# Performance work log

Measured on AMD Instinct MI355X. Metric: run time of the kernel, lower is better.

Reference implementation:

```python
import jax, jax.numpy as jnp
import numpy as np

IN_FEATURES = 4096
OUT_FEATURES = 4096
BLOCK_SIZE = 16
E2M1_VALUES = jnp.array([0.0, 0.5, 1.0, 1.5, 2.0, 3.0, 4.0, 6.0], dtype=jnp.float32)


def dequantize_nvfp4(weight_packed, weight_scales, out_features, in_features, block_size, dtype):
    # Unpack two 4-bit codes per byte: even positions = high nibble, odd = low nibble
    p = weight_packed.astype(jnp.int32)
    high = (p >> 4) & 15
    low = p & 15
    unpacked = jnp.stack([high, low], axis=-1).reshape(-1)  # [out*in]
    sign = ((unpacked >> 3) & 1).astype(dtype)
    mag_code = unpacked & 7
    magnitude = E2M1_VALUES.astype(dtype)[mag_code]
    vals = jnp.where(sign == 1, -magnitude, magnitude)
    # Expand per-block E4M3 scales (repeat_interleave)
    scales_expanded = jnp.repeat(weight_scales.astype(dtype), block_size)
    w = vals * scales_expanded
    return w.reshape(out_features, in_features)


def setup_inputs() -> dict:
    key = jax.random.key(0)
    k1, k2, k3, k4 = jax.random.split(key, 4)
    x = jax.random.normal(k1, (4, 2048, IN_FEATURES), dtype=jnp.float32)
    weight_packed = jax.random.randint(k2, (OUT_FEATURES * IN_FEATURES // 2,), 0, 256, dtype=jnp.int32)
    weight_scales = jax.random.uniform(k3, (OUT_FEATURES * IN_FEATURES // BLOCK_SIZE,), dtype=jnp.float32)
    bias = jax.random.normal(k4, (OUT_FEATURES,), dtype=jnp.float32)
    return {"x": x, "weight_packed": weight_packed, "weight_scales": weight_scales, "bias": bias}


def reference(x, weight_packed, weight_scales, bias):
    w = dequantize_nvfp4(weight_packed, weight_scales, OUT_FEATURES, IN_FEATURES, BLOCK_SIZE, x.dtype)
    # F.linear: y = x @ w.T + bias
    return jnp.einsum('bsi,oi->bso', x, w) + bias
```

## Files before the change

### kernel.cpp

```cpp
#include <hip/hip_runtime.h>
#include <cstdint>
#include <cstddef>

#define MDIM 8192
#define NDIM 4096
#define KDIM 4096

typedef __attribute__((ext_vector_type(8))) __bf16 bf16x8;
typedef __attribute__((ext_vector_type(4))) float floatx4;

typedef __attribute__((address_space(3))) void lds_t;
typedef __attribute__((address_space(1))) void glb_t;

__device__ __forceinline__ unsigned short f32_to_bf16(float f) {
  unsigned int u = __float_as_uint(f);
  u += 0x7FFFu + ((u >> 16) & 1u);
  return (unsigned short)(u >> 16);
}

__device__ __forceinline__ float fp4_mag(int c) {
  int e = (c >> 1) & 3, m = c & 1;
  int sh = e ? (e - 1) : 0;
  return e ? 0.5f * (float)((2 + m) << sh) : 0.5f * (float)m;
}

__global__ __launch_bounds__(256) void conv_x_kernel(const float* __restrict__ x,
                                                     unsigned short* __restrict__ xb) {
  const int t = blockIdx.x * 256 + threadIdx.x;
  const float4* src = (const float4*)x + (size_t)t * 2;
  float4 a = src[0], b = src[1];
  union { unsigned short us[8]; uint4 u4; } o;
  o.us[0] = f32_to_bf16(a.x); o.us[1] = f32_to_bf16(a.y);
  o.us[2] = f32_to_bf16(a.z); o.us[3] = f32_to_bf16(a.w);
  o.us[4] = f32_to_bf16(b.x); o.us[5] = f32_to_bf16(b.y);
  o.us[6] = f32_to_bf16(b.z); o.us[7] = f32_to_bf16(b.w);
  ((uint4*)xb)[t] = o.u4;
}

__global__ __launch_bounds__(256) void dequant_kernel(const int* __restrict__ packed,
                                                      const float* __restrict__ scales,
                                                      unsigned short* __restrict__ wb) {
  const int t = blockIdx.x * 256 + threadIdx.x;
  const int4* p = (const int4*)packed + (size_t)t * 2;
  int4 pa = p[0], pb = p[1];
  float s = scales[t];
  int bytes[8] = {pa.x, pa.y, pa.z, pa.w, pb.x, pb.y, pb.z, pb.w};
  union { unsigned short us[16]; uint4 u4[2]; } o;
#pragma unroll
  for (int i = 0; i < 8; ++i) {
    int by = bytes[i] & 255;
    int hi = by >> 4, lo = by & 15;
    float vh = fp4_mag(hi & 7) * s; if (hi & 8) vh = -vh;
    float vl = fp4_mag(lo & 7) * s; if (lo & 8) vl = -vl;
    o.us[2 * i]     = f32_to_bf16(vh);
    o.us[2 * i + 1] = f32_to_bf16(vl);
  }
  uint4* dst = (uint4*)(wb + (size_t)t * 16);
  dst[0] = o.u4[0]; dst[1] = o.u4[1];
}

__global__ __launch_bounds__(256, 3) void gemm_kernel(const __bf16* __restrict__ A,
                                                      const __bf16* __restrict__ B,
                                                      const float* __restrict__ bias,
                                                      float* __restrict__ C) {
  __shared__ __bf16 As[128 * 32];
  __shared__ __bf16 Bs[128 * 32];
  const int t = threadIdx.x;
  const int wave = t >> 6, lane = t & 63;
  const int quad = lane >> 4, r16 = lane & 15;
  const int wm = (wave >> 1) * 64, wn = (wave & 1) * 64;
  const int m0 = blockIdx.y * 128, n0 = blockIdx.x * 128;

  floatx4 acc[4][4] = {};

  const int sr = t >> 2;
  const int sc = (t & 3) * 8;

  const __bf16* ga = A + (size_t)(m0 + sr) * KDIM + sc;
  const __bf16* gb = B + (size_t)(n0 + sr) * KDIM + sc;

  for (int k0 = 0; k0 < KDIM; k0 += 32) {
    __builtin_amdgcn_global_load_lds((const glb_t*)(ga),
                                     (lds_t*)(As + wave * 512), 16, 0, 0);
    __builtin_amdgcn_global_load_lds((const glb_t*)(ga + (size_t)64 * KDIM),
                                     (lds_t*)(As + 2048 + wave * 512), 16, 0, 0);
    __builtin_amdgcn_global_load_lds((const glb_t*)(gb),
                                     (lds_t*)(Bs + wave * 512), 16, 0, 0);
    __builtin_amdgcn_global_load_lds((const glb_t*)(gb + (size_t)64 * KDIM),
                                     (lds_t*)(Bs + 2048 + wave * 512), 16, 0, 0);
    ga += 32; gb += 32;
    __syncthreads();

    bf16x8 af[4], bfr[4];
#pragma unroll
    for (int i = 0; i < 4; ++i) {
      af[i]  = *(const bf16x8*)(As + (wm + i * 16 + r16) * 32 + quad * 8);
      bfr[i] = *(const bf16x8*)(Bs + (wn + i * 16 + r16) * 32 + quad * 8);
    }
#pragma unroll
    for (int i = 0; i < 4; ++i)
#pragma unroll
      for (int j = 0; j < 4; ++j)
        acc[i][j] = __builtin_amdgcn_mfma_f32_16x16x32_bf16(af[i], bfr[j], acc[i][j], 0, 0, 0);
    __syncthreads();
  }

  float bv[4];
#pragma unroll
  for (int j = 0; j < 4; ++j) bv[j] = bias[n0 + wn + j * 16 + r16];
#pragma unroll
  for (int i = 0; i < 4; ++i) {
    const int gm = m0 + wm + i * 16 + quad * 4;
#pragma unroll
    for (int j = 0; j < 4; ++j) {
      float* cp = C + (size_t)gm * NDIM + (n0 + wn + j * 16 + r16);
#pragma unroll
      for (int r = 0; r < 4; ++r)
        cp[(size_t)r * NDIM] = acc[i][j][r] + bv[j];
    }
  }
}

__global__ __launch_bounds__(256) void fused_fallback(const float* __restrict__ x,
                                                      const int* __restrict__ packed,
                                                      const float* __restrict__ scales,
                                                      const float* __restrict__ bias,
                                                      float* __restrict__ out) {
  const int n = blockIdx.x * 256 + threadIdx.x;
  const int m = blockIdx.y;
  const float* xr = x + (size_t)m * KDIM;
  const int* pr = packed + (size_t)n * (KDIM / 2);
  const float* sc = scales + (size_t)n * (KDIM / 16);
  float acc = 0.f;
  for (int kb = 0; kb < KDIM / 16; ++kb) {
    float s = sc[kb];
    float part = 0.f;
#pragma unroll
    for (int i = 0; i < 8; ++i) {
      int by = pr[kb * 8 + i] & 255;
      int hi = by >> 4, lo = by & 15;
      float vh = fp4_mag(hi & 7); if (hi & 8) vh = -vh;
      float vl = fp4_mag(lo & 7); if (lo & 8) vl = -vl;
      part += xr[kb * 16 + 2 * i] * vh + xr[kb * 16 + 2 * i + 1] * vl;
    }
    acc += s * part;
  }
  out[(size_t)m * NDIM + n] = acc + bias[n];
}

extern "C" void kernel_launch(void* const* d_in, const int* in_sizes, int n_in,
                              void* d_out, int out_size, void* d_ws, size_t ws_size,
                              hipStream_t stream) {
  const float* x      = (const float*)d_in[0];
  const int*   packed = (const int*)d_in[1];
  const float* scales = (const float*)d_in[2];
  const float* bias   = (const float*)d_in[3];
  float* out = (float*)d_out;

  const size_t needA = (size_t)MDIM * KDIM * 2;
  const size_t needW = (size_t)NDIM * KDIM * 2;

  if (ws_size >= needA + needW) {
    unsigned short* xb = (unsigned short*)d_ws;
    unsigned short* wb = (unsigned short*)((char*)d_ws + needA);
    conv_x_kernel<<<(MDIM * KDIM / 8) / 256, 256, 0, stream>>>(x, xb);
    dequant_kernel<<<(NDIM * KDIM / 16) / 256, 256, 0, stream>>>(packed, scales, wb);
    dim3 grid(NDIM / 128, MDIM / 128);
    gemm_kernel<<<grid, 256, 0, stream>>>((const __bf16*)xb, (const __bf16*)wb, bias, out);
  } else {
    dim3 grid(NDIM / 256, MDIM);
    fused_fallback<<<grid, 256, 0, stream>>>(x, packed, scales, bias, out);
  }
}
```

Measured before the change: 546.8 us.

## Switch GEMM to 32x32x16 MFMA tiles and merge prep kernels into one launch

The GEMM now uses 32x32x16 bf16 MFMA instructions with a 2x2 accumulator grid per wave instead of 4x4 16x16x32 tiles. This cuts the number of MFMA issues and LDS fragment loads per K step. The x conversion and weight dequant kernels are merged into a single launch, and each thread now handles twice as much data, which removes one kernel launch. The 32x32 output layout changes the store pattern, giving less coalesced writes per lane row.

```diff
diff --git a/kernel.cpp b/kernel.cpp
--- a/kernel.cpp
+++ b/kernel.cpp
@@ -7,7 +7,7 @@
 #define KDIM 4096
 
 typedef __attribute__((ext_vector_type(8))) __bf16 bf16x8;
-typedef __attribute__((ext_vector_type(4))) float floatx4;
+typedef __attribute__((ext_vector_type(16))) float floatx16;
 
 typedef __attribute__((address_space(3))) void lds_t;
 typedef __attribute__((address_space(1))) void glb_t;
@@ -24,39 +24,47 @@
   return e ? 0.5f * (float)((2 + m) << sh) : 0.5f * (float)m;
 }
 
-__global__ __launch_bounds__(256) void conv_x_kernel(const float* __restrict__ x,
-                                                     unsigned short* __restrict__ xb) {
-  const int t = blockIdx.x * 256 + threadIdx.x;
-  const float4* src = (const float4*)x + (size_t)t * 2;
-  float4 a = src[0], b = src[1];
-  union { unsigned short us[8]; uint4 u4; } o;
-  o.us[0] = f32_to_bf16(a.x); o.us[1] = f32_to_bf16(a.y);
-  o.us[2] = f32_to_bf16(a.z); o.us[3] = f32_to_bf16(a.w);
-  o.us[4] = f32_to_bf16(b.x); o.us[5] = f32_to_bf16(b.y);
-  o.us[6] = f32_to_bf16(b.z); o.us[7] = f32_to_bf16(b.w);
-  ((uint4*)xb)[t] = o.u4;
-}
-
-__global__ __launch_bounds__(256) void dequant_kernel(const int* __restrict__ packed,
-                                                      const float* __restrict__ scales,
-                                                      unsigned short* __restrict__ wb) {
-  const int t = blockIdx.x * 256 + threadIdx.x;
-  const int4* p = (const int4*)packed + (size_t)t * 2;
-  int4 pa = p[0], pb = p[1];
-  float s = scales[t];
-  int bytes[8] = {pa.x, pa.y, pa.z, pa.w, pb.x, pb.y, pb.z, pb.w};
-  union { unsigned short us[16]; uint4 u4[2]; } o;
+__global__ __launch_bounds__(256) void prep_kernel(const float* __restrict__ x,
+                                                   unsigned short* __restrict__ xb,
+                                                   const int* __restrict__ packed,
+                                                   const float* __restrict__ scales,
+                                                   unsigned short* __restrict__ wb) {
+  if (blockIdx.x < 8192) {
+    const int t = blockIdx.x * 256 + threadIdx.x;
+    const float4* src = (const float4*)x + (size_t)t * 4;
+    float4 a = src[0], b = src[1], c = src[2], d = src[3];
+    union { unsigned short us[16]; uint4 u4[2]; } o;
+    o.us[0]  = f32_to_bf16(a.x); o.us[1]  = f32_to_bf16(a.y);
+    o.us[2]  = f32_to_bf16(a.z); o.us[3]  = f32_to_bf16(a.w);
+    o.us[4]  = f32_to_bf16(b.x); o.us[5]  = f32_to_bf16(b.y);
+    o.us[6]  = f32_to_bf16(b.z); o.us[7]  = f32_to_bf16(b.w);
+    o.us[8]  = f32_to_bf16(c.x); o.us[9]  = f32_to_bf16(c.y);
+    o.us[10] = f32_to_bf16(c.z); o.us[11] = f32_to_bf16(c.w);
+    o.us[12] = f32_to_bf16(d.x); o.us[13] = f32_to_bf16(d.y);
+    o.us[14] = f32_to_bf16(d.z); o.us[15] = f32_to_bf16(d.w);
+    uint4* dst = (uint4*)xb + (size_t)t * 2;
+    dst[0] = o.u4[0]; dst[1] = o.u4[1];
+  } else {
+    const int u = (blockIdx.x - 8192) * 256 + threadIdx.x;
+    const int4* p = (const int4*)packed + (size_t)u * 4;
+    int4 p0 = p[0], p1 = p[1], p2 = p[2], p3 = p[3];
+    float s0 = scales[2 * u], s1 = scales[2 * u + 1];
+    int bytes[16] = {p0.x, p0.y, p0.z, p0.w, p1.x, p1.y, p1.z, p1.w,
+                     p2.x, p2.y, p2.z, p2.w, p3.x, p3.y, p3.z, p3.w};
+    union { unsigned short us[32]; uint4 u4[4]; } o;
 #pragma unroll
-  for (int i = 0; i < 8; ++i) {
-    int by = bytes[i] & 255;
-    int hi = by >> 4, lo = by & 15;
-    float vh = fp4_mag(hi & 7) * s; if (hi & 8) vh = -vh;
-    float vl = fp4_mag(lo & 7) * s; if (lo & 8) vl = -vl;
-    o.us[2 * i]     = f32_to_bf16(vh);
-    o.us[2 * i + 1] = f32_to_bf16(vl);
+    for (int i = 0; i < 16; ++i) {
+      float s = (i < 8) ? s0 : s1;
+      int by = bytes[i] & 255;
+      int hi = by >> 4, lo = by & 15;
+      float vh = fp4_mag(hi & 7) * s; if (hi & 8) vh = -vh;
+      float vl = fp4_mag(lo & 7) * s; if (lo & 8) vl = -vl;
+      o.us[2 * i]     = f32_to_bf16(vh);
+      o.us[2 * i + 1] = f32_to_bf16(vl);
+    }
+    uint4* dst = (uint4*)wb + (size_t)u * 4;
+    dst[0] = o.u4[0]; dst[1] = o.u4[1]; dst[2] = o.u4[2]; dst[3] = o.u4[3];
   }
-  uint4* dst = (uint4*)(wb + (size_t)t * 16);
-  dst[0] = o.u4[0]; dst[1] = o.u4[1];
 }
 
 __global__ __launch_bounds__(256, 3) void gemm_kernel(const __bf16* __restrict__ A,
@@ -67,11 +75,11 @@
   __shared__ __bf16 Bs[128 * 32];
   const int t = threadIdx.x;
   const int wave = t >> 6, lane = t & 63;
-  const int quad = lane >> 4, r16 = lane & 15;
+  const int r32 = lane & 31, half = lane >> 5;
   const int wm = (wave >> 1) * 64, wn = (wave & 1) * 64;
   const int m0 = blockIdx.y * 128, n0 = blockIdx.x * 128;
 
-  floatx4 acc[4][4] = {};
+  floatx16 acc[2][2] = {};
 
   const int sr = t >> 2;
   const int sc = (t & 3) * 8;
@@ -91,34 +99,37 @@
     ga += 32; gb += 32;
     __syncthreads();
 
-    bf16x8 af[4], bfr[4];
 #pragma unroll
-    for (int i = 0; i < 4; ++i) {
-      af[i]  = *(const bf16x8*)(As + (wm + i * 16 + r16) * 32 + quad * 8);
-      bfr[i] = *(const bf16x8*)(Bs + (wn + i * 16 + r16) * 32 + quad * 8);
+    for (int kh = 0; kh < 2; ++kh) {
+      bf16x8 af[2], bfr[2];
+#pragma unroll
+      for (int i = 0; i < 2; ++i) {
+        af[i]  = *(const bf16x8*)(As + (wm + i * 32 + r32) * 32 + kh * 16 + half * 8);
+        bfr[i] = *(const bf16x8*)(Bs + (wn + i * 32 + r32) * 32 + kh * 16 + half * 8);
+      }
+#pragma unroll
+      for (int i = 0; i < 2; ++i)
+#pragma unroll
+        for (int j = 0; j < 2; ++j)
+          acc[i][j] = __builtin_amdgcn_mfma_f32_32x32x16_bf16(af[i], bfr[j], acc[i][j], 0, 0, 0);
     }
-#pragma unroll
-    for (int i = 0; i < 4; ++i)
-#pragma unroll
-      for (int j = 0; j < 4; ++j)
-        acc[i][j] = __builtin_amdgcn_mfma_f32_16x16x32_bf16(af[i], bfr[j], acc[i][j], 0, 0, 0);
     __syncthreads();
   }
 
-  float bv[4];
+  float bv[2];
 #pragma unroll
-  for (int j = 0; j < 4; ++j) bv[j] = bias[n0 + wn + j * 16 + r16];
+  for (int j = 0; j < 2; ++j) bv[j] = bias[n0 + wn + j * 32 + r32];
 #pragma unroll
-  for (int i = 0; i < 4; ++i) {
-    const int gm = m0 + wm + i * 16 + quad * 4;
+  for (int i = 0; i < 2; ++i)
 #pragma unroll
-    for (int j = 0; j < 4; ++j) {
-      float* cp = C + (size_t)gm * NDIM + (n0 + wn + j * 16 + r16);
+    for (int j = 0; j < 2; ++j) {
+      const int gc = n0 + wn + j * 32 + r32;
 #pragma unroll
-      for (int r = 0; r < 4; ++r)
-        cp[(size_t)r * NDIM] = acc[i][j][r] + bv[j];
+      for (int r = 0; r < 16; ++r) {
+        const int gr = m0 + wm + i * 32 + (r & 3) + 8 * (r >> 2) + 4 * half;
+        C[(size_t)gr * NDIM + gc] = acc[i][j][r] + bv[j];
+      }
     }
-  }
 }
 
 __global__ __launch_bounds__(256) void fused_fallback(const float* __restrict__ x,
@@ -163,8 +174,7 @@
   if (ws_size >= needA + needW) {
     unsigned short* xb = (unsigned short*)d_ws;
     unsigned short* wb = (unsigned short*)((char*)d_ws + needA);
-    conv_x_kernel<<<(MDIM * KDIM / 8) / 256, 256, 0, stream>>>(x, xb);
-    dequant_kernel<<<(NDIM * KDIM / 16) / 256, 256, 0, stream>>>(packed, scales, wb);
+    prep_kernel<<<10240, 256, 0, stream>>>(x, xb, packed, scales, wb);
     dim3 grid(NDIM / 128, MDIM / 128);
     gemm_kernel<<<grid, 256, 0, stream>>>((const __bf16*)xb, (const __bf16*)wb, bias, out);
   } else {
```

Measured after the change: 587.8 us. 7.5% more time.

## Fuse fp32-to-bf16 activation conversion into GEMM tile loading

Applied to the files above, without the earlier changes.

Removes the separate conversion kernel for x and has the GEMM stream fp32 activations directly into LDS via global_load_lds. The fp32 A tile uses an XOR swizzle on 16-byte chunks, and each lane converts two float4 reads to a bf16x8 fragment before the MFMA. This saves the extra write and read of the bf16 copy of x, but doubles A-tile global traffic inside the GEMM, doubles A's LDS footprint, and adds conversion ALU work in the inner loop.

```diff
diff --git a/kernel.cpp b/kernel.cpp
--- a/kernel.cpp
+++ b/kernel.cpp
@@ -24,19 +24,6 @@
   return e ? 0.5f * (float)((2 + m) << sh) : 0.5f * (float)m;
 }
 
-__global__ __launch_bounds__(256) void conv_x_kernel(const float* __restrict__ x,
-                                                     unsigned short* __restrict__ xb) {
-  const int t = blockIdx.x * 256 + threadIdx.x;
-  const float4* src = (const float4*)x + (size_t)t * 2;
-  float4 a = src[0], b = src[1];
-  union { unsigned short us[8]; uint4 u4; } o;
-  o.us[0] = f32_to_bf16(a.x); o.us[1] = f32_to_bf16(a.y);
-  o.us[2] = f32_to_bf16(a.z); o.us[3] = f32_to_bf16(a.w);
-  o.us[4] = f32_to_bf16(b.x); o.us[5] = f32_to_bf16(b.y);
-  o.us[6] = f32_to_bf16(b.z); o.us[7] = f32_to_bf16(b.w);
-  ((uint4*)xb)[t] = o.u4;
-}
-
 __global__ __launch_bounds__(256) void dequant_kernel(const int* __restrict__ packed,
                                                       const float* __restrict__ scales,
                                                       unsigned short* __restrict__ wb) {
@@ -59,11 +46,11 @@
   dst[0] = o.u4[0]; dst[1] = o.u4[1];
 }
 
-__global__ __launch_bounds__(256, 3) void gemm_kernel(const __bf16* __restrict__ A,
+__global__ __launch_bounds__(256, 3) void gemm_kernel(const float* __restrict__ A,
                                                       const __bf16* __restrict__ B,
                                                       const float* __restrict__ bias,
                                                       float* __restrict__ C) {
-  __shared__ __bf16 As[128 * 32];
+  __shared__ float As[128 * 32];
   __shared__ __bf16 Bs[128 * 32];
   const int t = threadIdx.x;
   const int wave = t >> 6, lane = t & 63;
@@ -73,17 +60,21 @@
 
   floatx4 acc[4][4] = {};
 
+  const int ar = t >> 3;
+  const int ac = ((t & 7) ^ (ar & 7)) * 4;
+  const float* ga = A + (size_t)(m0 + ar) * KDIM + ac;
+
   const int sr = t >> 2;
   const int sc = (t & 3) * 8;
-
-  const __bf16* ga = A + (size_t)(m0 + sr) * KDIM + sc;
   const __bf16* gb = B + (size_t)(n0 + sr) * KDIM + sc;
 
+  const int c0 = ((quad * 2) ^ (r16 & 7));
+
   for (int k0 = 0; k0 < KDIM; k0 += 32) {
-    __builtin_amdgcn_global_load_lds((const glb_t*)(ga),
-                                     (lds_t*)(As + wave * 512), 16, 0, 0);
-    __builtin_amdgcn_global_load_lds((const glb_t*)(ga + (size_t)64 * KDIM),
-                                     (lds_t*)(As + 2048 + wave * 512), 16, 0, 0);
+#pragma unroll
+    for (int q = 0; q < 4; ++q)
+      __builtin_amdgcn_global_load_lds((const glb_t*)(ga + (size_t)q * 32 * KDIM),
+                                       (lds_t*)(As + q * 1024 + wave * 256), 16, 0, 0);
     __builtin_amdgcn_global_load_lds((const glb_t*)(gb),
                                      (lds_t*)(Bs + wave * 512), 16, 0, 0);
     __builtin_amdgcn_global_load_lds((const glb_t*)(gb + (size_t)64 * KDIM),
@@ -94,7 +85,15 @@
     bf16x8 af[4], bfr[4];
 #pragma unroll
     for (int i = 0; i < 4; ++i) {
-      af[i]  = *(const bf16x8*)(As + (wm + i * 16 + r16) * 32 + quad * 8);
+      const float* arow = As + (wm + i * 16 + r16) * 32;
+      floatx4 f0 = *(const floatx4*)(arow + c0 * 4);
+      floatx4 f1 = *(const floatx4*)(arow + (c0 ^ 1) * 4);
+      bf16x8 a;
+      a[0] = (__bf16)f0[0]; a[1] = (__bf16)f0[1];
+      a[2] = (__bf16)f0[2]; a[3] = (__bf16)f0[3];
+      a[4] = (__bf16)f1[0]; a[5] = (__bf16)f1[1];
+      a[6] = (__bf16)f1[2]; a[7] = (__bf16)f1[3];
+      af[i] = a;
       bfr[i] = *(const bf16x8*)(Bs + (wn + i * 16 + r16) * 32 + quad * 8);
     }
 #pragma unroll
@@ -157,16 +156,13 @@
   const float* bias   = (const float*)d_in[3];
   float* out = (float*)d_out;
 
-  const size_t needA = (size_t)MDIM * KDIM * 2;
   const size_t needW = (size_t)NDIM * KDIM * 2;
 
-  if (ws_size >= needA + needW) {
-    unsigned short* xb = (unsigned short*)d_ws;
-    unsigned short* wb = (unsigned short*)((char*)d_ws + needA);
-    conv_x_kernel<<<(MDIM * KDIM / 8) / 256, 256, 0, stream>>>(x, xb);
+  if (ws_size >= needW) {
+    unsigned short* wb = (unsigned short*)d_ws;
     dequant_kernel<<<(NDIM * KDIM / 16) / 256, 256, 0, stream>>>(packed, scales, wb);
     dim3 grid(NDIM / 128, MDIM / 128);
-    gemm_kernel<<<grid, 256, 0, stream>>>((const __bf16*)xb, (const __bf16*)wb, bias, out);
+    gemm_kernel<<<grid, 256, 0, stream>>>(x, (const __bf16*)wb, bias, out);
   } else {
     dim3 grid(NDIM / 256, MDIM);
     fused_fallback<<<grid, 256, 0, stream>>>(x, packed, scales, bias, out);
```

Result: slower. 630.9 us (+15.4%).
